# Kernel tuning notes

Measured on AMD Instinct MI355X. Metric: run time of the kernel, lower is better.

## Reference

```python
import jax, jax.numpy as jnp
import numpy as np

N_NODES = 50000
N_EDGES = 400000
N_GRAPHS = 64
HEADS = 4
GAT_DIM = 128
Z_DIM = 128
NEG_SLOPE = 0.2


def _glorot(key, shape):
    fan_in, fan_out = shape[0], shape[1]
    lim = (6.0 / (fan_in + fan_out)) ** 0.5
    return jax.random.uniform(key, shape, jnp.float32, -lim, lim)


def setup_inputs() -> dict:
    key = jax.random.key(0)
    ks = jax.random.split(key, 32)
    inp = {}
    inp['x'] = jax.random.normal(ks[0], (N_NODES, 3), jnp.float32)
    inp['edge_index'] = jax.random.randint(ks[1], (2, N_EDGES), 0, N_NODES, jnp.int64)
    inp['batch'] = jnp.sort(jax.random.randint(ks[2], (N_NODES,), 0, N_GRAPHS, jnp.int64))
    in_dims = [3, GAT_DIM, GAT_DIM]
    ki = 3
    for l, d_in in enumerate(in_dims):
        inp[f'Wl{l}'] = _glorot(ks[ki], (d_in, HEADS * GAT_DIM)); ki += 1
        inp[f'bl{l}'] = jnp.zeros((HEADS * GAT_DIM,), jnp.float32)
        inp[f'Wr{l}'] = _glorot(ks[ki], (d_in, HEADS * GAT_DIM)); ki += 1
        inp[f'br{l}'] = jnp.zeros((HEADS * GAT_DIM,), jnp.float32)
        inp[f'att{l}'] = _glorot(ks[ki], (HEADS, GAT_DIM)); ki += 1
        inp[f'b{l}'] = jnp.zeros((GAT_DIM,), jnp.float32)
    inp['lin_W'] = _glorot(ks[ki], (GAT_DIM, Z_DIM)); ki += 1
    inp['lin_b'] = jnp.zeros((Z_DIM,), jnp.float32)
    return inp


def gatv2_conv(x, src, dst, Wl, bl, Wr, br, att, bias):
    N = x.shape[0]
    xl = (x @ Wl + bl).reshape(N, HEADS, GAT_DIM)  # source transform
    xr = (x @ Wr + br).reshape(N, HEADS, GAT_DIM)  # target transform
    m = xl[src] + xr[dst]                           # [E,H,C]
    e = jnp.einsum('ehc,hc->eh', jax.nn.leaky_relu(m, NEG_SLOPE), att)  # [E,H]
    # segment softmax over incoming edges of each target node
    emax = jax.ops.segment_max(e, dst, num_segments=N)
    ee = jnp.exp(e - emax[dst])
    denom = jax.ops.segment_sum(ee, dst, num_segments=N)
    alpha = ee / denom[dst]                         # [E,H]
    out = jax.ops.segment_sum(alpha[:, :, None] * xl[src], dst, num_segments=N)  # [N,H,C]
    return out.mean(axis=1) + bias                  # concat=False -> head mean


def reference(x, edge_index, batch,
              Wl0, bl0, Wr0, br0, att0, b0,
              Wl1, bl1, Wr1, br1, att1, b1,
              Wl2, bl2, Wr2, br2, att2, b2,
              lin_W, lin_b):
    src, dst = edge_index[0], edge_index[1]
    params = [(Wl0, bl0, Wr0, br0, att0, b0),
              (Wl1, bl1, Wr1, br1, att1, b1),
              (Wl2, bl2, Wr2, br2, att2, b2)]
    h = x
    for (Wl, bl, Wr, br, att, b) in params:
        h = jax.nn.elu(gatv2_conv(h, src, dst, Wl, bl, Wr, br, att, b))
    # global mean pool over graphs
    sums = jax.ops.segment_sum(h, batch, num_segments=N_GRAPHS)
    cnt = jax.ops.segment_sum(jnp.ones((h.shape[0],), h.dtype), batch, num_segments=N_GRAPHS)
    g = sums / jnp.maximum(cnt, 1.0)[:, None]
    return g @ lin_W + lin_b
```

## Files before the change

### kernel.cpp

```cpp
#include <hip/hip_runtime.h>
#include <hip/hip_bf16.h>
#include <hip/hip_fp16.h>

#define N_NODES 50000
#define N_EDGES 400000
#define N_GRAPHS 64
#define HEADS 4
#define GAT_DIM 128
#define FDIM 512
#define NEG_SLOPE 0.2f

#define A6C 0.8656170245333781f
#define A4C 0.5770780163555854f

#define DPP_ADD(x, ctrl) ((x) + __int_as_float(__builtin_amdgcn_mov_dpp( \
        __float_as_int(x), (ctrl), 0xF, 0xF, true)))

typedef _Float16 f16x8 __attribute__((ext_vector_type(8)));
typedef float f32x4 __attribute__((ext_vector_type(4)));

__global__ void deg_kernel(const int* __restrict__ edst, int* __restrict__ deg) {
    int e = blockIdx.x * blockDim.x + threadIdx.x;
    if (e < N_EDGES) atomicAdd(&deg[edst[e]], 1);
}

__global__ __launch_bounds__(1024) void scan_kernel(const int* __restrict__ deg,
                                                    int* __restrict__ off) {
    __shared__ int part[1024];
    const int n = N_NODES;
    int t = threadIdx.x;
    int chunk = (n + 1023) / 1024;
    int base = t * chunk;
    int s = 0;
    for (int i = 0; i < chunk; i++) {
        int idx = base + i;
        if (idx < n) s += deg[idx];
    }
    part[t] = s;
    __syncthreads();
    for (int d = 1; d < 1024; d <<= 1) {
        int add = (t >= d) ? part[t - d] : 0;
        __syncthreads();
        part[t] += add;
        __syncthreads();
    }
    int run = part[t] - s;
    for (int i = 0; i < chunk; i++) {
        int idx = base + i;
        if (idx < n) { off[idx] = run; run += deg[idx]; }
    }
    if (t == 0) off[n] = part[1023];
}

__global__ void fill_kernel(const int* __restrict__ esrc, const int* __restrict__ edst,
                            const int* __restrict__ off, int* __restrict__ cursor,
                            int* __restrict__ csr_src) {
    int e = blockIdx.x * blockDim.x + threadIdx.x;
    if (e >= N_EDGES) return;
    int d = edst[e];
    int pos = off[d] + atomicAdd(&cursor[d], 1);
    csr_src[pos] = esrc[e];
}

__global__ __launch_bounds__(128) void wprep_kernel(const float* __restrict__ Wl,
                                                    const float* __restrict__ Wr,
                                                    const float* __restrict__ bl,
                                                    const float* __restrict__ br,
                                                    __half* __restrict__ Wt,
                                                    float* __restrict__ bc) {
    int n = blockIdx.x;
    int k = threadIdx.x;
    float v = (n < 512) ? Wl[(size_t)k * 512 + n] : Wr[(size_t)k * 512 + (n - 512)];
    Wt[(size_t)n * 128 + k] = __float2half(v);
    if (k == 0) bc[n] = (n < 512) ? bl[n] : br[n - 512];
}

#define GM 64
#define GP 132
__global__ __launch_bounds__(256) void gemm_mfma_kernel(const __half* __restrict__ A,
                                                        const __half* __restrict__ Wt,
                                                        const float* __restrict__ bc,
                                                        __half* __restrict__ xl,
                                                        __half* __restrict__ xr, int M) {
    __shared__ __align__(16) _Float16 As[GM * GP];
    __shared__ __align__(16) _Float16 Bs[128 * GP];
    const int bm = blockIdx.x * GM;
    const int tid = threadIdx.x;

#pragma unroll
    for (int i = 0; i < 4; i++) {
        int ci = tid + 256 * i;
        int r = ci >> 4;
        int k8 = (ci & 15) * 8;
        int gr = bm + r;
        f16x8 v;
        if (gr < M) {
            v = *(const f16x8*)(A + (size_t)gr * 128 + k8);
        } else {
            v = (f16x8){(_Float16)0, (_Float16)0, (_Float16)0, (_Float16)0,
                        (_Float16)0, (_Float16)0, (_Float16)0, (_Float16)0};
        }
        *(f16x8*)&As[r * GP + k8] = v;
    }

    const int wid = tid >> 6, lane = tid & 63;
    const int wm = wid & 1, wn = wid >> 1;
    const int lm = lane & 15;
    const int lk = (lane >> 4) * 8;
    const int lr4 = (lane >> 4) * 4;

    for (int cb = 0; cb < 8; cb++) {
        __syncthreads();
#pragma unroll
        for (int i = 0; i < 8; i++) {
            int ci = tid + 256 * i;
            int r = ci >> 4;
            int k8 = (ci & 15) * 8;
            *(f16x8*)&Bs[r * GP + k8] =
                *(const f16x8*)(Wt + ((size_t)(cb * 128 + r)) * 128 + k8);
        }
        __syncthreads();

        f32x4 acc[4][2];
#pragma unroll
        for (int fn = 0; fn < 4; fn++)
#pragma unroll
            for (int fm = 0; fm < 2; fm++) acc[fn][fm] = (f32x4){0.f, 0.f, 0.f, 0.f};

#pragma unroll
        for (int ks = 0; ks < 4; ks++) {
            f16x8 af[4], bf[2];
#pragma unroll
            for (int fn = 0; fn < 4; fn++)
                af[fn] = *(const f16x8*)&Bs[(wn * 64 + fn * 16 + lm) * GP + ks * 32 + lk];
#pragma unroll
            for (int fm = 0; fm < 2; fm++)
                bf[fm] = *(const f16x8*)&As[(wm * 32 + fm * 16 + lm) * GP + ks * 32 + lk];
#pragma unroll
            for (int fn = 0; fn < 4; fn++)
#pragma unroll
                for (int fm = 0; fm < 2; fm++)
                    acc[fn][fm] = __builtin_amdgcn_mfma_f32_16x16x32_f16(af[fn], bf[fm],
                                                                         acc[fn][fm], 0, 0, 0);
        }
        __syncthreads();

        _Float16* Cs = Bs;
#pragma unroll
        for (int fn = 0; fn < 4; fn++) {
            float4 b4 = *(const float4*)(bc + cb * 128 + wn * 64 + fn * 16 + lr4);
#pragma unroll
            for (int fm = 0; fm < 2; fm++) {
                f32x4 v = acc[fn][fm];
                union { _Float16 h[4]; float2 f2; } u;
                u.h[0] = (_Float16)(v[0] + b4.x);
                u.h[1] = (_Float16)(v[1] + b4.y);
                u.h[2] = (_Float16)(v[2] + b4.z);
                u.h[3] = (_Float16)(v[3] + b4.w);
                int m_loc = wm * 32 + fm * 16 + lm;
                int n_loc = wn * 64 + fn * 16 + lr4;
                *(float2*)&Cs[m_loc * GP + n_loc] = u.f2;
            }
        }
        __syncthreads();

        __half* dst = (cb < 4) ? xl : xr;
        const int c0 = (cb & 3) * 128;
#pragma unroll
        for (int i = 0; i < 4; i++) {
            int ci = tid + 256 * i;
            int r = ci >> 4;
            int c8 = (ci & 15) * 8;
            int gr = bm + r;
            if (gr < M) {
                float4 v = *(const float4*)&Cs[r * GP + c8];
                *(float4*)(dst + (size_t)gr * 512 + c0 + c8) = v;
            }
        }
    }
}

#define EW0_BLOCKS 2048
#define EW0_NW (EW0_BLOCKS * 4)
__global__ __launch_bounds__(256) void fused_edge0_kernel(const int* __restrict__ off,
                                                          const int* __restrict__ csr_src,
                                                          const float* __restrict__ x,
                                                          const float* __restrict__ Wl,
                                                          const float* __restrict__ bl,
                                                          const float* __restrict__ Wr,
                                                          const float* __restrict__ br,
                                                          const float* __restrict__ att,
                                                          const float* __restrict__ bias,
                                                          __half* __restrict__ hout) {
    const int lane = threadIdx.x & 63;
    const int wglob = blockIdx.x * 4 + (threadIdx.x >> 6);
    const int loff = lane * 8;
    float4 wl00 = *(const float4*)(Wl + loff),        wl01 = *(const float4*)(Wl + loff + 4);
    float4 wl10 = *(const float4*)(Wl + 512 + loff),  wl11 = *(const float4*)(Wl + 512 + loff + 4);
    float4 wl20 = *(const float4*)(Wl + 1024 + loff), wl21 = *(const float4*)(Wl + 1024 + loff + 4);
    float4 bl0  = *(const float4*)(bl + loff),        bl1  = *(const float4*)(bl + loff + 4);
    float4 at0  = *(const float4*)(att + loff),       at1  = *(const float4*)(att + loff + 4);
    float4 wr00 = *(const float4*)(Wr + loff),        wr01 = *(const float4*)(Wr + loff + 4);
    float4 wr10 = *(const float4*)(Wr + 512 + loff),  wr11 = *(const float4*)(Wr + 512 + loff + 4);
    float4 wr20 = *(const float4*)(Wr + 1024 + loff), wr21 = *(const float4*)(Wr + 1024 + loff + 4);
    float4 br0  = *(const float4*)(br + loff),        br1  = *(const float4*)(br + loff + 4);

    for (int n = wglob; n < N_NODES; n += EW0_NW) {
        int s = off[n], e = off[n + 1];
        float xn0 = x[n * 3 + 0], xn1 = x[n * 3 + 1], xn2 = x[n * 3 + 2];
        float4 xr0, xr1;
        xr0.x = fmaf(xn0, wr00.x, fmaf(xn1, wr10.x, fmaf(xn2, wr20.x, br0.x)));
        xr0.y = fmaf(xn0, wr00.y, fmaf(xn1, wr10.y, fmaf(xn2, wr20.y, br0.y)));
        xr0.z = fmaf(xn0, wr00.z, fmaf(xn1, wr10.z, fmaf(xn2, wr20.z, br0.z)));
        xr0.w = fmaf(xn0, wr00.w, fmaf(xn1, wr10.w, fmaf(xn2, wr20.w, br0.w)));
        xr1.x = fmaf(xn0, wr01.x, fmaf(xn1, wr11.x, fmaf(xn2, wr21.x, br1.x)));
        xr1.y = fmaf(xn0, wr01.y, fmaf(xn1, wr11.y, fmaf(xn2, wr21.y, br1.y)));
        xr1.z = fmaf(xn0, wr01.z, fmaf(xn1, wr11.z, fmaf(xn2, wr21.z, br1.z)));
        xr1.w = fmaf(xn0, wr01.w, fmaf(xn1, wr11.w, fmaf(xn2, wr21.w, br1.w)));

        float mx = -1e30f, denom = 0.f;
        float a0 = 0.f, a1 = 0.f, a2 = 0.f, a3 = 0.f, a4 = 0.f, a5 = 0.f, a6 = 0.f, a7 = 0.f;

        float c0, c1, c2, n0, n1, n2;
        if (s < e) { int i0 = csr_src[s]; c0 = x[i0 * 3]; c1 = x[i0 * 3 + 1]; c2 = x[i0 * 3 + 2]; }
        if (s + 1 < e) { int i1 = csr_src[s + 1]; n0 = x[i1 * 3]; n1 = x[i1 * 3 + 1]; n2 = x[i1 * 3 + 2]; }
        for (int p = s; p < e; p++) {
            float t0, t1, t2;
            if (p + 2 < e) {
                int i2 = csr_src[p + 2];
                t0 = x[i2 * 3]; t1 = x[i2 * 3 + 1]; t2 = x[i2 * 3 + 2];
            }
            float4 v0, v1;
            v0.x = fmaf(c0, wl00.x, fmaf(c1, wl10.x, fmaf(c2, wl20.x, bl0.x)));
            v0.y = fmaf(c0, wl00.y, fmaf(c1, wl10.y, fmaf(c2, wl20.y, bl0.y)));
            v0.z = fmaf(c0, wl00.z, fmaf(c1, wl10.z, fmaf(c2, wl20.z, bl0.z)));
            v0.w = fmaf(c0, wl00.w, fmaf(c1, wl10.w, fmaf(c2, wl20.w, bl0.w)));
            v1.x = fmaf(c0, wl01.x, fmaf(c1, wl11.x, fmaf(c2, wl21.x, bl1.x)));
            v1.y = fmaf(c0, wl01.y, fmaf(c1, wl11.y, fmaf(c2, wl21.y, bl1.y)));
            v1.z = fmaf(c0, wl01.z, fmaf(c1, wl11.z, fmaf(c2, wl21.z, bl1.z)));
            v1.w = fmaf(c0, wl01.w, fmaf(c1, wl11.w, fmaf(c2, wl21.w, bl1.w)));
            float mm, s1, s2;
            mm = v0.x + xr0.x; s1 = at0.x * mm; s2 = at0.x * fabsf(mm);
            mm = v0.y + xr0.y; s1 = fmaf(at0.y, mm, s1); s2 = fmaf(at0.y, fabsf(mm), s2);
            mm = v0.z + xr0.z; s1 = fmaf(at0.z, mm, s1); s2 = fmaf(at0.z, fabsf(mm), s2);
            mm = v0.w + xr0.w; s1 = fmaf(at0.w, mm, s1); s2 = fmaf(at0.w, fabsf(mm), s2);
            mm = v1.x + xr1.x; s1 = fmaf(at1.x, mm, s1); s2 = fmaf(at1.x, fabsf(mm), s2);
            mm = v1.y + xr1.y; s1 = fmaf(at1.y, mm, s1); s2 = fmaf(at1.y, fabsf(mm), s2);
            mm = v1.z + xr1.z; s1 = fmaf(at1.z, mm, s1); s2 = fmaf(at1.z, fabsf(mm), s2);
            mm = v1.w + xr1.w; s1 = fmaf(at1.w, mm, s1); s2 = fmaf(at1.w, fabsf(mm), s2);
            float part = fmaf(A6C, s1, A4C * s2);
            part = DPP_ADD(part, 0xB1);
            part = DPP_ADD(part, 0x4E);
            part = DPP_ADD(part, 0x124);
            part = DPP_ADD(part, 0x128);
            float mnew = fmaxf(mx, part);
            float scale = exp2f(mx - mnew);
            float w = exp2f(part - mnew);
            denom = fmaf(denom, scale, w);
            a0 = fmaf(a0, scale, w * v0.x);
            a1 = fmaf(a1, scale, w * v0.y);
            a2 = fmaf(a2, scale, w * v0.z);
            a3 = fmaf(a3, scale, w * v0.w);
            a4 = fmaf(a4, scale, w * v1.x);
            a5 = fmaf(a5, scale, w * v1.y);
            a6 = fmaf(a6, scale, w * v1.z);
            a7 = fmaf(a7, scale, w * v1.w);
            mx = mnew;
            c0 = n0; c1 = n1; c2 = n2;
            n0 = t0; n1 = t1; n2 = t2;
        }
        float inv = denom > 0.f ? 1.f / denom : 0.f;
        a0 *= inv; a1 *= inv; a2 *= inv; a3 *= inv;
        a4 *= inv; a5 *= inv; a6 *= inv; a7 *= inv;
        a0 += __shfl_xor(a0, 16); a0 += __shfl_xor(a0, 32);
        a1 += __shfl_xor(a1, 16); a1 += __shfl_xor(a1, 32);
        a2 += __shfl_xor(a2, 16); a2 += __shfl_xor(a2, 32);
        a3 += __shfl_xor(a3, 16); a3 += __shfl_xor(a3, 32);
        a4 += __shfl_xor(a4, 16); a4 += __shfl_xor(a4, 32);
        a5 += __shfl_xor(a5, 16); a5 += __shfl_xor(a5, 32);
        a6 += __shfl_xor(a6, 16); a6 += __shfl_xor(a6, 32);
        a7 += __shfl_xor(a7, 16); a7 += __shfl_xor(a7, 32);
        if (lane < 16) {
            float4 b0 = *(const float4*)(bias + lane * 8);
            float4 b1 = *(const float4*)(bias + lane * 8 + 4);
            float o[8];
            o[0] = fmaf(0.25f, a0, b0.x); o[1] = fmaf(0.25f, a1, b0.y);
            o[2] = fmaf(0.25f, a2, b0.z); o[3] = fmaf(0.25f, a3, b0.w);
            o[4] = fmaf(0.25f, a4, b1.x); o[5] = fmaf(0.25f, a5, b1.y);
            o[6] = fmaf(0.25f, a6, b1.z); o[7] = fmaf(0.25f, a7, b1.w);
#pragma unroll
            for (int j = 0; j < 8; j++) o[j] = o[j] > 0.f ? o[j] : (__expf(o[j]) - 1.f);
            union { __half2 h2[4]; float4 f4; } u;
            u.h2[0] = __float22half2_rn(make_float2(o[0], o[1]));
            u.h2[1] = __float22half2_rn(make_float2(o[2], o[3]));
            u.h2[2] = __float22half2_rn(make_float2(o[4], o[5]));
            u.h2[3] = __float22half2_rn(make_float2(o[6], o[7]));
            *(float4*)(hout + (size_t)n * GAT_DIM + lane * 8) = u.f4;
        }
    }
}

__global__ __launch_bounds__(256) void fused_edge_kernel(const int* __restrict__ off,
                                                         const int* __restrict__ csr_src,
                                                         const __half* __restrict__ xl,
                                                         const __half* __restrict__ xr,
                                                         const float* __restrict__ att,
                                                         const float* __restrict__ bias,
                                                         __half* __restrict__ hout) {
    int wid = threadIdx.x >> 6;
    int lane = threadIdx.x & 63;
    int n = blockIdx.x * 4 + wid;
    if (n >= N_NODES) return;
    int s = off[n], e = off[n + 1];
    const int loff = lane * 8;
    float4 xr0, xr1;
    {
        float4 rxr = *(const float4*)(xr + (size_t)n * FDIM + loff);
        const __half2* xp = (const __half2*)&rxr;
        float2 x01 = __half22float2(xp[0]);
        float2 x23 = __half22float2(xp[1]);
        float2 x45 = __half22float2(xp[2]);
        float2 x67 = __half22float2(xp[3]);
        xr0 = make_float4(x01.x, x01.y, x23.x, x23.y);
        xr1 = make_float4(x45.x, x45.y, x67.x, x67.y);
    }
    float4 at0 = *(const float4*)(att + loff);
    float4 at1 = *(const float4*)(att + loff + 4);

    float mx = -1e30f, denom = 0.f;
    float a0 = 0.f, a1 = 0.f, a2 = 0.f, a3 = 0.f, a4 = 0.f, a5 = 0.f, a6 = 0.f, a7 = 0.f;

    float4 rcur, rnext;
    if (s < e)     rcur  = *(const float4*)(xl + (size_t)csr_src[s] * FDIM + loff);
    if (s + 1 < e) rnext = *(const float4*)(xl + (size_t)csr_src[s + 1] * FDIM + loff);
    for (int p = s; p < e; p++) {
        float4 rt;
        if (p + 2 < e) rt = *(const float4*)(xl + (size_t)csr_src[p + 2] * FDIM + loff);
        float4 v0, v1;
        {
            const __half2* hp = (const __half2*)&rcur;
            float2 f01 = __half22float2(hp[0]);
            float2 f23 = __half22float2(hp[1]);
            float2 f45 = __half22float2(hp[2]);
            float2 f67 = __half22float2(hp[3]);
            v0 = make_float4(f01.x, f01.y, f23.x, f23.y);
            v1 = make_float4(f45.x, f45.y, f67.x, f67.y);
        }
        float mm, s1, s2;
        mm = v0.x + xr0.x; s1 = at0.x * mm; s2 = at0.x * fabsf(mm);
        mm = v0.y + xr0.y; s1 = fmaf(at0.y, mm, s1); s2 = fmaf(at0.y, fabsf(mm), s2);
        mm = v0.z + xr0.z; s1 = fmaf(at0.z, mm, s1); s2 = fmaf(at0.z, fabsf(mm), s2);
        mm = v0.w + xr0.w; s1 = fmaf(at0.w, mm, s1); s2 = fmaf(at0.w, fabsf(mm), s2);
        mm = v1.x + xr1.x; s1 = fmaf(at1.x, mm, s1); s2 = fmaf(at1.x, fabsf(mm), s2);
        mm = v1.y + xr1.y; s1 = fmaf(at1.y, mm, s1); s2 = fmaf(at1.y, fabsf(mm), s2);
        mm = v1.z + xr1.z; s1 = fmaf(at1.z, mm, s1); s2 = fmaf(at1.z, fabsf(mm), s2);
        mm = v1.w + xr1.w; s1 = fmaf(at1.w, mm, s1); s2 = fmaf(at1.w, fabsf(mm), s2);
        float part = fmaf(A6C, s1, A4C * s2);
        part = DPP_ADD(part, 0xB1);
        part = DPP_ADD(part, 0x4E);
        part = DPP_ADD(part, 0x124);
        part = DPP_ADD(part, 0x128);
        float mnew = fmaxf(mx, part);
        float scale = exp2f(mx - mnew);
        float w = exp2f(part - mnew);
        denom = fmaf(denom, scale, w);
        a0 = fmaf(a0, scale, w * v0.x);
        a1 = fmaf(a1, scale, w * v0.y);
        a2 = fmaf(a2, scale, w * v0.z);
        a3 = fmaf(a3, scale, w * v0.w);
        a4 = fmaf(a4, scale, w * v1.x);
        a5 = fmaf(a5, scale, w * v1.y);
        a6 = fmaf(a6, scale, w * v1.z);
        a7 = fmaf(a7, scale, w * v1.w);
        mx = mnew;
        rcur = rnext;
        rnext = rt;
    }
    float inv = denom > 0.f ? 1.f / denom : 0.f;
    a0 *= inv; a1 *= inv; a2 *= inv; a3 *= inv;
    a4 *= inv; a5 *= inv; a6 *= inv; a7 *= inv;
    a0 += __shfl_xor(a0, 16); a0 += __shfl_xor(a0, 32);
    a1 += __shfl_xor(a1, 16); a1 += __shfl_xor(a1, 32);
    a2 += __shfl_xor(a2, 16); a2 += __shfl_xor(a2, 32);
    a3 += __shfl_xor(a3, 16); a3 += __shfl_xor(a3, 32);
    a4 += __shfl_xor(a4, 16); a4 += __shfl_xor(a4, 32);
    a5 += __shfl_xor(a5, 16); a5 += __shfl_xor(a5, 32);
    a6 += __shfl_xor(a6, 16); a6 += __shfl_xor(a6, 32);
    a7 += __shfl_xor(a7, 16); a7 += __shfl_xor(a7, 32);
    if (lane < 16) {
        float4 b0 = *(const float4*)(bias + lane * 8);
        float4 b1 = *(const float4*)(bias + lane * 8 + 4);
        float o[8];
        o[0] = fmaf(0.25f, a0, b0.x); o[1] = fmaf(0.25f, a1, b0.y);
        o[2] = fmaf(0.25f, a2, b0.z); o[3] = fmaf(0.25f, a3, b0.w);
        o[4] = fmaf(0.25f, a4, b1.x); o[5] = fmaf(0.25f, a5, b1.y);
        o[6] = fmaf(0.25f, a6, b1.z); o[7] = fmaf(0.25f, a7, b1.w);
#pragma unroll
        for (int j = 0; j < 8; j++) o[j] = o[j] > 0.f ? o[j] : (__expf(o[j]) - 1.f);
        union { __half2 h2[4]; float4 f4; } u;
        u.h2[0] = __float22half2_rn(make_float2(o[0], o[1]));
        u.h2[1] = __float22half2_rn(make_float2(o[2], o[3]));
        u.h2[2] = __float22half2_rn(make_float2(o[4], o[5]));
        u.h2[3] = __float22half2_rn(make_float2(o[6], o[7]));
        *(float4*)(hout + (size_t)n * GAT_DIM + lane * 8) = u.f4;
    }
}

#define POOL_CHUNK 64
__global__ __launch_bounds__(128) void pool_kernel(const __half* __restrict__ h,
                                                   const int* __restrict__ batch,
                                                   double* __restrict__ psum,
                                                   int* __restrict__ pcnt) {
    int c = threadIdx.x;
    int n0 = blockIdx.x * POOL_CHUNK;
    int n1 = min(n0 + POOL_CHUNK, N_NODES);
    if (n0 >= N_NODES) return;
    double acc = 0.0;
    int cur = batch[n0];
    int cnt = 0;
    for (int n = n0; n < n1; n++) {
        int g = batch[n];
        if (g != cur) {
            atomicAdd(&psum[(size_t)cur * GAT_DIM + c], acc);
            if (c == 0) atomicAdd(&pcnt[cur], cnt);
            acc = 0.0; cnt = 0; cur = g;
        }
        acc += (double)__half2float(h[(size_t)n * GAT_DIM + c]);
        cnt++;
    }
    atomicAdd(&psum[(size_t)cur * GAT_DIM + c], acc);
    if (c == 0) atomicAdd(&pcnt[cur], cnt);
}

__global__ __launch_bounds__(128) void final_kernel(const double* __restrict__ psum,
                                                    const int* __restrict__ pcnt,
                                                    const float* __restrict__ linW,
                                                    const float* __restrict__ linb,
                                                    float* __restrict__ out) {
    int g = blockIdx.x;
    int j = threadIdx.x;
    __shared__ float gv[128];
    float cnt = (float)max(pcnt[g], 1);
    gv[j] = (float)(psum[(size_t)g * 128 + j] / (double)cnt);
    __syncthreads();
    float acc = 0.f;
    for (int c = 0; c < 128; c++) acc = fmaf(gv[c], linW[c * 128 + j], acc);
    out[(size_t)g * 128 + j] = acc + linb[j];
}

extern "C" void kernel_launch(void* const* d_in, const int* in_sizes, int n_in,
                              void* d_out, int out_size, void* d_ws, size_t ws_size,
                              hipStream_t stream) {
    const float* x    = (const float*)d_in[0];
    const int* eidx   = (const int*)d_in[1];
    const int* batch  = (const int*)d_in[2];
    const float* Wl[3] = {(const float*)d_in[3],  (const float*)d_in[9],  (const float*)d_in[15]};
    const float* bl[3] = {(const float*)d_in[4],  (const float*)d_in[10], (const float*)d_in[16]};
    const float* Wr[3] = {(const float*)d_in[5],  (const float*)d_in[11], (const float*)d_in[17]};
    const float* br[3] = {(const float*)d_in[6],  (const float*)d_in[12], (const float*)d_in[18]};
    const float* att[3] = {(const float*)d_in[7], (const float*)d_in[13], (const float*)d_in[19]};
    const float* bb[3] = {(const float*)d_in[8],  (const float*)d_in[14], (const float*)d_in[20]};
    const float* linW = (const float*)d_in[21];
    const float* linb = (const float*)d_in[22];
    float* out = (float*)d_out;

    const int* esrc = eidx;
    const int* edst = eidx + N_EDGES;

    char* p = (char*)d_ws;
    auto alloc = [&](size_t bytes) { void* r = (void*)p; p += (bytes + 255) & ~(size_t)255; return r; };
    __half* xl     = (__half*)alloc((size_t)N_NODES * FDIM * 2);
    __half* xr     = (__half*)alloc((size_t)N_NODES * FDIM * 2);
    __half* hbuf   = (__half*)alloc((size_t)N_NODES * GAT_DIM * 2);
    int*   off     = (int*)alloc((size_t)(N_NODES + 1) * 4);
    int*   csr_src = (int*)alloc((size_t)N_EDGES * 4);
    __half* Wt1    = (__half*)alloc((size_t)1024 * 128 * 2);
    __half* Wt2    = (__half*)alloc((size_t)1024 * 128 * 2);
    float* bc1     = (float*)alloc((size_t)1024 * 4);
    float* bc2     = (float*)alloc((size_t)1024 * 4);
    char* zbase = p;
    int*   deg     = (int*)alloc((size_t)N_NODES * 4);
    int*   cursor  = (int*)alloc((size_t)N_NODES * 4);
    double* psum   = (double*)alloc((size_t)N_GRAPHS * GAT_DIM * 8);
    int*   pcnt    = (int*)alloc((size_t)N_GRAPHS * 4);
    size_t zbytes = (size_t)(p - zbase);

    hipMemsetAsync(zbase, 0, zbytes, stream);

    deg_kernel<<<(N_EDGES + 255) / 256, 256, 0, stream>>>(edst, deg);
    scan_kernel<<<1, 1024, 0, stream>>>(deg, off);
    fill_kernel<<<(N_EDGES + 255) / 256, 256, 0, stream>>>(esrc, edst, off, cursor, csr_src);
    wprep_kernel<<<1024, 128, 0, stream>>>(Wl[1], Wr[1], bl[1], br[1], Wt1, bc1);
    wprep_kernel<<<1024, 128, 0, stream>>>(Wl[2], Wr[2], bl[2], br[2], Wt2, bc2);

    const int ggrid = (N_NODES + GM - 1) / GM;
    const int egrid = (N_NODES + 3) / 4;

    fused_edge0_kernel<<<EW0_BLOCKS, 256, 0, stream>>>(off, csr_src, x, Wl[0], bl[0],
                                                       Wr[0], br[0], att[0], bb[0], hbuf);
    __half* Wt[3] = {nullptr, Wt1, Wt2};
    float*  bc[3] = {nullptr, bc1, bc2};
    for (int l = 1; l < 3; l++) {
        gemm_mfma_kernel<<<ggrid, 256, 0, stream>>>(hbuf, Wt[l], bc[l], xl, xr, N_NODES);
        fused_edge_kernel<<<egrid, 256, 0, stream>>>(off, csr_src, xl, xr,
                                                     att[l], bb[l], hbuf);
    }

    pool_kernel<<<(N_NODES + POOL_CHUNK - 1) / POOL_CHUNK, 128, 0, stream>>>(hbuf, batch, psum, pcnt);
    final_kernel<<<N_GRAPHS, 128, 0, stream>>>(psum, pcnt, linW, linb, out);
}
```

Before: 592.8 us.

## Parallelize degree scan across blocks, merge weight prep launches, use exp2 in ELU

Result: faster. 512.0 us (-13.6%).

```diff
diff --git a/kernel.cpp b/kernel.cpp
--- a/kernel.cpp
+++ b/kernel.cpp
@@ -12,6 +12,7 @@
 
 #define A6C 0.8656170245333781f
 #define A4C 0.5770780163555854f
+#define L2E 1.4426950408889634f
 
 #define DPP_ADD(x, ctrl) ((x) + __int_as_float(__builtin_amdgcn_mov_dpp( \
         __float_as_int(x), (ctrl), 0xF, 0xF, true)))
@@ -24,32 +25,51 @@
     if (e < N_EDGES) atomicAdd(&deg[edst[e]], 1);
 }
 
-__global__ __launch_bounds__(1024) void scan_kernel(const int* __restrict__ deg,
+#define SCB 256
+#define SCNB ((N_NODES + SCB - 1) / SCB)
+__global__ __launch_bounds__(SCB) void scan1_kernel(const int* __restrict__ deg,
+                                                    int* __restrict__ bsum) {
+    __shared__ int sm[SCB];
+    int n = blockIdx.x * SCB + threadIdx.x;
+    sm[threadIdx.x] = (n < N_NODES) ? deg[n] : 0;
+    __syncthreads();
+    for (int d = SCB / 2; d > 0; d >>= 1) {
+        if (threadIdx.x < d) sm[threadIdx.x] += sm[threadIdx.x + d];
+        __syncthreads();
+    }
+    if (threadIdx.x == 0) bsum[blockIdx.x] = sm[0];
+}
+__global__ __launch_bounds__(SCB) void scan2_kernel(int* __restrict__ bsum,
                                                     int* __restrict__ off) {
-    __shared__ int part[1024];
-    const int n = N_NODES;
+    __shared__ int sm[SCB];
     int t = threadIdx.x;
-    int chunk = (n + 1023) / 1024;
-    int base = t * chunk;
-    int s = 0;
-    for (int i = 0; i < chunk; i++) {
-        int idx = base + i;
-        if (idx < n) s += deg[idx];
-    }
-    part[t] = s;
+    int v = (t < SCNB) ? bsum[t] : 0;
+    sm[t] = v;
     __syncthreads();
-    for (int d = 1; d < 1024; d <<= 1) {
-        int add = (t >= d) ? part[t - d] : 0;
-        __syncthreads();
-        part[t] += add;
-        __syncthreads();
-    }
-    int run = part[t] - s;
-    for (int i = 0; i < chunk; i++) {
-        int idx = base + i;
-        if (idx < n) { off[idx] = run; run += deg[idx]; }
-    }
-    if (t == 0) off[n] = part[1023];
+    for (int d = 1; d < SCB; d <<= 1) {
+        int add = (t >= d) ? sm[t - d] : 0;
+        __syncthreads();
+        sm[t] += add;
+        __syncthreads();
+    }
+    if (t < SCNB) bsum[t] = sm[t] - v;
+    if (t == SCNB - 1) off[N_NODES] = sm[t];
+}
+__global__ __launch_bounds__(SCB) void scan3_kernel(const int* __restrict__ deg,
+                                                    const int* __restrict__ bsum,
+                                                    int* __restrict__ off) {
+    __shared__ int sm[SCB];
+    int n = blockIdx.x * SCB + threadIdx.x;
+    int v = (n < N_NODES) ? deg[n] : 0;
+    sm[threadIdx.x] = v;
+    __syncthreads();
+    for (int d = 1; d < SCB; d <<= 1) {
+        int add = (threadIdx.x >= d) ? sm[threadIdx.x - d] : 0;
+        __syncthreads();
+        sm[threadIdx.x] += add;
+        __syncthreads();
+    }
+    if (n < N_NODES) off[n] = bsum[blockIdx.x] + sm[threadIdx.x] - v;
 }
 
 __global__ void fill_kernel(const int* __restrict__ esrc, const int* __restrict__ edst,
@@ -62,14 +82,27 @@
     csr_src[pos] = esrc[e];
 }
 
-__global__ __launch_bounds__(128) void wprep_kernel(const float* __restrict__ Wl,
-                                                    const float* __restrict__ Wr,
-                                                    const float* __restrict__ bl,
-                                                    const float* __restrict__ br,
-                                                    __half* __restrict__ Wt,
-                                                    float* __restrict__ bc) {
-    int n = blockIdx.x;
+__global__ __launch_bounds__(128) void wprep_kernel(const float* __restrict__ Wl1,
+                                                    const float* __restrict__ Wr1,
+                                                    const float* __restrict__ bl1,
+                                                    const float* __restrict__ br1,
+                                                    const float* __restrict__ Wl2,
+                                                    const float* __restrict__ Wr2,
+                                                    const float* __restrict__ bl2,
+                                                    const float* __restrict__ br2,
+                                                    __half* __restrict__ Wt1,
+                                                    float* __restrict__ bc1,
+                                                    __half* __restrict__ Wt2,
+                                                    float* __restrict__ bc2) {
+    int b = blockIdx.x;
     int k = threadIdx.x;
+    const float* Wl = (b < 1024) ? Wl1 : Wl2;
+    const float* Wr = (b < 1024) ? Wr1 : Wr2;
+    const float* bl = (b < 1024) ? bl1 : bl2;
+    const float* br = (b < 1024) ? br1 : br2;
+    __half* Wt = (b < 1024) ? Wt1 : Wt2;
+    float* bc = (b < 1024) ? bc1 : bc2;
+    int n = b & 1023;
     float v = (n < 512) ? Wl[(size_t)k * 512 + n] : Wr[(size_t)k * 512 + (n - 512)];
     Wt[(size_t)n * 128 + k] = __float2half(v);
     if (k == 0) bc[n] = (n < 512) ? bl[n] : br[n - 512];
@@ -289,7 +322,7 @@
             o[4] = fmaf(0.25f, a4, b1.x); o[5] = fmaf(0.25f, a5, b1.y);
             o[6] = fmaf(0.25f, a6, b1.z); o[7] = fmaf(0.25f, a7, b1.w);
 #pragma unroll
-            for (int j = 0; j < 8; j++) o[j] = o[j] > 0.f ? o[j] : (__expf(o[j]) - 1.f);
+            for (int j = 0; j < 8; j++) o[j] = o[j] > 0.f ? o[j] : (exp2f(o[j] * L2E) - 1.f);
             union { __half2 h2[4]; float4 f4; } u;
             u.h2[0] = __float22half2_rn(make_float2(o[0], o[1]));
             u.h2[1] = __float22half2_rn(make_float2(o[2], o[3]));
@@ -396,7 +429,7 @@
         o[4] = fmaf(0.25f, a4, b1.x); o[5] = fmaf(0.25f, a5, b1.y);
         o[6] = fmaf(0.25f, a6, b1.z); o[7] = fmaf(0.25f, a7, b1.w);
 #pragma unroll
-        for (int j = 0; j < 8; j++) o[j] = o[j] > 0.f ? o[j] : (__expf(o[j]) - 1.f);
+        for (int j = 0; j < 8; j++) o[j] = o[j] > 0.f ? o[j] : (exp2f(o[j] * L2E) - 1.f);
         union { __half2 h2[4]; float4 f4; } u;
         u.h2[0] = __float22half2_rn(make_float2(o[0], o[1]));
         u.h2[1] = __float22half2_rn(make_float2(o[2], o[3]));
@@ -474,6 +507,7 @@
     __half* hbuf   = (__half*)alloc((size_t)N_NODES * GAT_DIM * 2);
     int*   off     = (int*)alloc((size_t)(N_NODES + 1) * 4);
     int*   csr_src = (int*)alloc((size_t)N_EDGES * 4);
+    int*   bsum    = (int*)alloc((size_t)SCNB * 4);
     __half* Wt1    = (__half*)alloc((size_t)1024 * 128 * 2);
     __half* Wt2    = (__half*)alloc((size_t)1024 * 128 * 2);
     float* bc1     = (float*)alloc((size_t)1024 * 4);
@@ -488,10 +522,13 @@
     hipMemsetAsync(zbase, 0, zbytes, stream);
 
     deg_kernel<<<(N_EDGES + 255) / 256, 256, 0, stream>>>(edst, deg);
-    scan_kernel<<<1, 1024, 0, stream>>>(deg, off);
+    scan1_kernel<<<SCNB, SCB, 0, stream>>>(deg, bsum);
+    scan2_kernel<<<1, SCB, 0, stream>>>(bsum, off);
+    scan3_kernel<<<SCNB, SCB, 0, stream>>>(deg, bsum, off);
     fill_kernel<<<(N_EDGES + 255) / 256, 256, 0, stream>>>(esrc, edst, off, cursor, csr_src);
-    wprep_kernel<<<1024, 128, 0, stream>>>(Wl[1], Wr[1], bl[1], br[1], Wt1, bc1);
-    wprep_kernel<<<1024, 128, 0, stream>>>(Wl[2], Wr[2], bl[2], br[2], Wt2, bc2);
+    wprep_kernel<<<2048, 128, 0, stream>>>(Wl[1], Wr[1], bl[1], br[1],
+                                           Wl[2], Wr[2], bl[2], br[2],
+                                           Wt1, bc1, Wt2, bc2);
 
     const int ggrid = (N_NODES + GM - 1) / GM;
     const int egrid = (N_NODES + 3) / 4;
```
